# Performance work log

Hardware: AMD Instinct MI355X
Metric: run time of the kernel (lower is better)

The kernel has to match this reference:

```python
import jax, jax.numpy as jnp
import numpy as np

B, H, S, D = 4, 16, 2048, 64
NEG = -9e15


def setup_inputs() -> dict:
    key = jax.random.key(0)
    kq, kk, kv = jax.random.split(key, 3)
    q = jax.random.normal(kq, (B, H, S, D), dtype=jnp.float32)
    k = jax.random.normal(kk, (B, H, S, D), dtype=jnp.float32)
    v = jax.random.normal(kv, (B, H, S, D), dtype=jnp.float32)
    # causal mask: 1 where attention allowed, 0 where masked
    mask = jnp.tril(jnp.ones((S, S), dtype=jnp.int32))[None, None]
    return {"q": q, "k": k, "v": v, "mask": mask}


def reference(q, k, v, mask):
    d_k = q.shape[-1]
    # [B,H,S,S] scores
    scores = jnp.einsum("bhqd,bhkd->bhqk", q, k) / jnp.sqrt(jnp.float32(d_k))
    scores = jnp.where(mask == 0, jnp.float32(NEG), scores)
    attn = jax.nn.softmax(scores, axis=-1)
    return jnp.einsum("bhqk,bhkd->bhqd", attn, v)
```

## Files before the change

### kernel.cpp

```cpp
#include <hip/hip_runtime.h>

#define SLEN 2048
#define DH 64
#define NH 64
#define KVB 64
#define NT 32
#define NP 8
#define NEGBIG (-1e30f)
#define SCALE 0.18033688011112042f
#define DTHR 11.0f

typedef __attribute__((ext_vector_type(8))) short bf16x8;
typedef __attribute__((ext_vector_type(8))) unsigned short u16x8;
typedef __attribute__((ext_vector_type(16))) float f32x16;
typedef __attribute__((ext_vector_type(4))) unsigned int u32x4;

__device__ __forceinline__ ushort f2bf(float f) {
  union { float f; unsigned int u; } v; v.f = f;
  unsigned int r = v.u + 0x7fffu + ((v.u >> 16) & 1u);
  return (ushort)(r >> 16);
}

__device__ __forceinline__ unsigned int cvtpk(float lo, float hi2) {
  unsigned int r;
  asm("v_cvt_pk_bf16_f32 %0, %1, %2" : "=v"(r) : "v"(lo), "v"(hi2));
  return r;
}

__device__ __forceinline__ float xmaxh(float x) { return fmaxf(x, __shfl_xor(x, 32)); }
__device__ __forceinline__ float xsumh(float x) { return x + __shfl_xor(x, 32); }

__device__ __forceinline__ void gload16(const ushort* g, ushort* l) {
  __builtin_amdgcn_global_load_lds(
      (const __attribute__((address_space(1))) void*)g,
      (__attribute__((address_space(3))) void*)l, 16, 0, 0);
}

__global__ __launch_bounds__(256) void prep_k(const float* __restrict__ Kg,
                                              ushort* __restrict__ wsK) {
  const int tile = blockIdx.x, head = blockIdx.y, tid = threadIdx.x;
  const float* src = Kg + ((size_t)head * SLEN + (size_t)tile * KVB) * DH;
  ushort* dst = wsK + ((size_t)head * NT + tile) * (KVB * DH);
#pragma unroll
  for (int i = 0; i < 2; ++i) {
    const int id = tid + i * 256;
    const int r = id >> 3, c = id & 7;
    float4 a = *reinterpret_cast<const float4*>(src + r * DH + c * 8);
    float4 b = *reinterpret_cast<const float4*>(src + r * DH + c * 8 + 4);
    u16x8 t;
    t[0] = f2bf(a.x); t[1] = f2bf(a.y); t[2] = f2bf(a.z); t[3] = f2bf(a.w);
    t[4] = f2bf(b.x); t[5] = f2bf(b.y); t[6] = f2bf(b.z); t[7] = f2bf(b.w);
    *reinterpret_cast<u16x8*>(dst + r * DH + ((c ^ (r & 7)) * 8)) = t;
  }
}

__global__ __launch_bounds__(256) void prep_v(const float* __restrict__ Vg,
                                              ushort* __restrict__ wsV) {
  __shared__ float Vl[KVB][DH + 1];
  const int tile = blockIdx.x, head = blockIdx.y, tid = threadIdx.x;
  const float* src = Vg + ((size_t)head * SLEN + (size_t)tile * KVB) * DH;
#pragma unroll
  for (int i = 0; i < 4; ++i) {
    const int n = tid + i * 256;
    const int row = n >> 4, c4 = (n & 15) << 2;
    *reinterpret_cast<float4*>(&Vl[row][c4]) =
        *reinterpret_cast<const float4*>(src + row * DH + c4);
  }
  __syncthreads();
  ushort* dst = wsV + ((size_t)head * NT + tile) * (KVB * DH);
#pragma unroll
  for (int i = 0; i < 2; ++i) {
    const int id = tid + i * 256;
    const int d = id >> 3, c = id & 7;
    u16x8 t;
#pragma unroll
    for (int j = 0; j < 8; ++j) t[j] = f2bf(Vl[c * 8 + j][d]);
    *reinterpret_cast<u16x8*>(dst + d * DH + ((c ^ (d & 7)) * 8)) = t;
  }
}

__device__ __forceinline__ void strip_tile(
    const ushort* __restrict__ Kl, const ushort* __restrict__ Vl,
    const bf16x8* qf, f32x16& o0, f32x16& o1, float& m, float& l,
    int t, int tl, int q0, int ql, int hi) {
  f32x16 s0 = (f32x16)0.0f, s1 = (f32x16)0.0f;
#pragma unroll
  for (int ks = 0; ks < 4; ++ks) {
    const int c = ((ks * 2 + hi) ^ (ql & 7)) * 8;
    bf16x8 kf0 = *reinterpret_cast<const bf16x8*>(Kl + ql * 64 + c);
    bf16x8 kf1 = *reinterpret_cast<const bf16x8*>(Kl + (32 + ql) * 64 + c);
    s0 = __builtin_amdgcn_mfma_f32_32x32x16_bf16(kf0, qf[ks], s0, 0, 0, 0);
    s1 = __builtin_amdgcn_mfma_f32_32x32x16_bf16(kf1, qf[ks], s1, 0, 0, 0);
  }

  if (t == tl) {
    const int qg = q0 + ql;
#pragma unroll
    for (int r = 0; r < 16; ++r) {
      const int kr = t * 64 + (r & 3) + 8 * (r >> 2) + 4 * hi;
      if (kr > qg)      s0[r] = NEGBIG;
      if (kr + 32 > qg) s1[r] = NEGBIG;
    }
  }

  float tm[16];
#pragma unroll
  for (int r = 0; r < 16; ++r) tm[r] = fmaxf(s0[r], s1[r]);
#pragma unroll
  for (int st = 8; st >= 1; st >>= 1)
#pragma unroll
    for (int r = 0; r < 8; ++r)
      if (r < st) tm[r] = fmaxf(tm[r], tm[r + st]);
  const float pm = xmaxh(tm[0]);

  if (__any(pm > m + DTHR)) {
    const float mn = fmaxf(m, pm);
    const float sc = __builtin_exp2f(m - mn);
    m = mn;
    l *= sc;
#pragma unroll
    for (int r = 0; r < 16; ++r) { o0[r] *= sc; o1[r] *= sc; }
  }

#pragma unroll
  for (int r = 0; r < 16; ++r) s0[r] = __builtin_exp2f(s0[r] - m);
#pragma unroll
  for (int r = 0; r < 16; ++r) s1[r] = __builtin_exp2f(s1[r] - m);

  float ts[16];
#pragma unroll
  for (int r = 0; r < 16; ++r) ts[r] = s0[r] + s1[r];
#pragma unroll
  for (int st = 8; st >= 1; st >>= 1)
#pragma unroll
    for (int r = 0; r < 8; ++r)
      if (r < st) ts[r] += ts[r + st];
  l += xsumh(ts[0]);

  unsigned int pw0[8], pw1[8];
#pragma unroll
  for (int g = 0; g < 4; ++g)
#pragma unroll
    for (int j = 0; j < 2; ++j) {
      pw0[g * 2 + j] = cvtpk(s0[4 * g + 2 * j], s0[4 * g + 2 * j + 1]);
      pw1[g * 2 + j] = cvtpk(s1[4 * g + 2 * j], s1[4 * g + 2 * j + 1]);
    }

#pragma unroll
  for (int st = 0; st < 4; ++st) {
    const unsigned int* PW = (st < 2) ? pw0 : pw1;
    const int KH = st & 1;
    const unsigned int a0 = PW[4 * KH + 0], a1 = PW[4 * KH + 1];
    const unsigned int b0 = PW[4 * KH + 2], b1 = PW[4 * KH + 3];
    const unsigned int s0w = hi ? a0 : b0, s1w = hi ? a1 : b1;
    const unsigned int r0 = __shfl_xor(s0w, 32), r1 = __shfl_xor(s1w, 32);
    const unsigned int k0 = hi ? b0 : a0, k1 = hi ? b1 : a1;
    u32x4 fu;
    fu[0] = hi ? r0 : k0; fu[1] = hi ? r1 : k1;
    fu[2] = hi ? k0 : r0; fu[3] = hi ? k1 : r1;
    const bf16x8 pf = __builtin_bit_cast(bf16x8, fu);
    const int cv = ((st * 2 + hi) ^ (ql & 7)) * 8;
    const bf16x8 vf0 = *reinterpret_cast<const bf16x8*>(Vl + ql * 64 + cv);
    const bf16x8 vf1 = *reinterpret_cast<const bf16x8*>(Vl + (32 + ql) * 64 + cv);
    o0 = __builtin_amdgcn_mfma_f32_32x32x16_bf16(vf0, pf, o0, 0, 0, 0);
    o1 = __builtin_amdgcn_mfma_f32_32x32x16_bf16(vf1, pf, o1, 0, 0, 0);
  }
}

__device__ __forceinline__ void load_q(const float* Qh, int q0, int ql, int hi,
                                       bf16x8* qf) {
  const float* qrow = Qh + (size_t)(q0 + ql) * DH;
#pragma unroll
  for (int ks = 0; ks < 4; ++ks) {
    const int d0 = ks * 16 + hi * 8;
    float4 a = *reinterpret_cast<const float4*>(qrow + d0);
    float4 b = *reinterpret_cast<const float4*>(qrow + d0 + 4);
    bf16x8 t;
    t[0] = (short)f2bf(a.x * SCALE); t[1] = (short)f2bf(a.y * SCALE);
    t[2] = (short)f2bf(a.z * SCALE); t[3] = (short)f2bf(a.w * SCALE);
    t[4] = (short)f2bf(b.x * SCALE); t[5] = (short)f2bf(b.y * SCALE);
    t[6] = (short)f2bf(b.z * SCALE); t[7] = (short)f2bf(b.w * SCALE);
    qf[ks] = t;
  }
}

__device__ __forceinline__ void epi(float* Ow, float* Oh, const f32x16& o,
                                    float invl, int q0, int subd, int lane) {
  const int ql = lane & 31, hi = lane >> 5;
#pragma unroll
  for (int g = 0; g < 4; ++g) {
    float4 vv = make_float4(o[4 * g] * invl, o[4 * g + 1] * invl,
                            o[4 * g + 2] * invl, o[4 * g + 3] * invl);
    *reinterpret_cast<float4*>(Ow + ql * 36 + 8 * g + 4 * hi) = vv;
  }
#pragma unroll
  for (int i = 0; i < 4; ++i) {
    const int qr = (lane >> 3) + i * 8;
    const int c4 = (lane & 7) * 4;
    float4 vv = *reinterpret_cast<const float4*>(Ow + qr * 36 + c4);
    *reinterpret_cast<float4*>(Oh + (size_t)(q0 + qr) * DH + subd * 32 + c4) = vv;
  }
}

__global__ __launch_bounds__(256, 2) void attn_fwd5(
    const float* __restrict__ Qg, const ushort* __restrict__ wsK,
    const ushort* __restrict__ wsV, float* __restrict__ Og) {
  __shared__ __align__(16) float smem[8192];
  ushort* stg = (ushort*)smem;

  const int p    = blockIdx.x;
  const int head = blockIdx.y;
  const int tid  = threadIdx.x;
  const int w    = tid >> 6;
  const int lane = tid & 63;
  const int hi   = lane >> 5;
  const int ql   = lane & 31;

  const int q0A = p * 128 + w * 32;
  const int q0B = (15 - p) * 128 + w * 32;
  const int tlA = q0A >> 6;
  const int tlB = q0B >> 6;
  const int nt  = 32 - 2 * p;

  const float*  Qh    = Qg + (size_t)head * SLEN * DH;
  float*        Oh    = Og + (size_t)head * SLEN * DH;
  const ushort* kbase = wsK + (size_t)head * (NT * KVB * DH);
  const ushort* vbase = wsV + (size_t)head * (NT * KVB * DH);

#define STAGE(buf, t)                                                          \
  do {                                                                         \
    const size_t tb_ = (size_t)(t) * 4096;                                     \
    gload16(kbase + tb_ + tid * 8,        stg + (buf) * 8192 + tid * 8);       \
    gload16(kbase + tb_ + 2048 + tid * 8, stg + (buf) * 8192 + 2048 + tid * 8);\
    gload16(vbase + tb_ + tid * 8,        stg + (buf) * 8192 + 4096 + tid * 8);\
    gload16(vbase + tb_ + 2048 + tid * 8,                                      \
            stg + (buf) * 8192 + 6144 + tid * 8);                              \
  } while (0)

  STAGE(0, 0);

  bf16x8 qfA[4], qfB[4];
  load_q(Qh, q0A, ql, hi, qfA);
  load_q(Qh, q0B, ql, hi, qfB);

  f32x16 oA0 = (f32x16)0.0f, oA1 = (f32x16)0.0f;
  f32x16 oB0 = (f32x16)0.0f, oB1 = (f32x16)0.0f;
  float mA = -3.0e38f, lA = 0.0f, mB = -3.0e38f, lB = 0.0f;

  __syncthreads();

  int cur = 0;
  for (int t = 0; t < nt; ++t) {
    if (t + 1 < nt) STAGE(cur ^ 1, t + 1);

    const ushort* Kl = stg + cur * 8192;
    const ushort* Vl = Kl + 4096;

    if (t <= tlB) strip_tile(Kl, Vl, qfB, oB0, oB1, mB, lB, t, tlB, q0B, ql, hi);
    if (t <= tlA) strip_tile(Kl, Vl, qfA, oA0, oA1, mA, lA, t, tlA, q0A, ql, hi);

    __syncthreads();
    cur ^= 1;
  }
#undef STAGE

  float* Ow = smem + w * 1152;
  const float iA = 1.0f / lA, iB = 1.0f / lB;
  epi(Ow, Oh, oA0, iA, q0A, 0, lane);
  epi(Ow, Oh, oA1, iA, q0A, 1, lane);
  epi(Ow, Oh, oB0, iB, q0B, 0, lane);
  epi(Ow, Oh, oB1, iB, q0B, 1, lane);
}

extern "C" void kernel_launch(void* const* d_in, const int* in_sizes, int n_in,
                              void* d_out, int out_size, void* d_ws, size_t ws_size,
                              hipStream_t stream) {
  const float* q = (const float*)d_in[0];
  const float* k = (const float*)d_in[1];
  const float* v = (const float*)d_in[2];
  float* out = (float*)d_out;

  const size_t per = (size_t)NH * SLEN * DH;
  ushort* wsK = (ushort*)d_ws;
  ushort* wsV = wsK + per;

  prep_k<<<dim3(NT, NH), 256, 0, stream>>>(k, wsK);
  prep_v<<<dim3(NT, NH), 256, 0, stream>>>(v, wsV);
  attn_fwd5<<<dim3(NP, NH), 256, 0, stream>>>(q, wsK, wsV, out);
}
```

Measured before the change: 100.3 us.

## Split attention into 2-wave blocks with interleaved QK/softmax and MFMA priority

The attention kernel moves to 128-thread blocks, each covering a 64-row query strip paired with its mirrored strip, and launches twice as many blocks with head as the fast grid dimension. The per-tile work is split into a QK^T phase and a softmax+PV phase, so both strips' score MFMAs are issued before either softmax, and s_setprio raises wave priority around the MFMA sections. The intent is more parallelism and better overlap of matrix and vector work, at the cost of redundant K/V staging per block and extra live registers for two score tiles. The prep kernels swap grid axes to match.

```diff
diff --git a/kernel.cpp b/kernel.cpp
--- a/kernel.cpp
+++ b/kernel.cpp
@@ -5,7 +5,7 @@
 #define NH 64
 #define KVB 64
 #define NT 32
-#define NP 8
+#define NP 16
 #define NEGBIG (-1e30f)
 #define SCALE 0.18033688011112042f
 #define DTHR 11.0f
@@ -38,7 +38,7 @@
 
 __global__ __launch_bounds__(256) void prep_k(const float* __restrict__ Kg,
                                               ushort* __restrict__ wsK) {
-  const int tile = blockIdx.x, head = blockIdx.y, tid = threadIdx.x;
+  const int head = blockIdx.x, tile = blockIdx.y, tid = threadIdx.x;
   const float* src = Kg + ((size_t)head * SLEN + (size_t)tile * KVB) * DH;
   ushort* dst = wsK + ((size_t)head * NT + tile) * (KVB * DH);
 #pragma unroll
@@ -57,7 +57,7 @@
 __global__ __launch_bounds__(256) void prep_v(const float* __restrict__ Vg,
                                               ushort* __restrict__ wsV) {
   __shared__ float Vl[KVB][DH + 1];
-  const int tile = blockIdx.x, head = blockIdx.y, tid = threadIdx.x;
+  const int head = blockIdx.x, tile = blockIdx.y, tid = threadIdx.x;
   const float* src = Vg + ((size_t)head * SLEN + (size_t)tile * KVB) * DH;
 #pragma unroll
   for (int i = 0; i < 4; ++i) {
@@ -79,11 +79,11 @@
   }
 }
 
-__device__ __forceinline__ void strip_tile(
-    const ushort* __restrict__ Kl, const ushort* __restrict__ Vl,
-    const bf16x8* qf, f32x16& o0, f32x16& o1, float& m, float& l,
-    int t, int tl, int q0, int ql, int hi) {
-  f32x16 s0 = (f32x16)0.0f, s1 = (f32x16)0.0f;
+__device__ __forceinline__ void qkt(const ushort* __restrict__ Kl,
+                                    const bf16x8* qf, f32x16& s0, f32x16& s1,
+                                    int ql, int hi) {
+  s0 = (f32x16)0.0f; s1 = (f32x16)0.0f;
+  __builtin_amdgcn_s_setprio(1);
 #pragma unroll
   for (int ks = 0; ks < 4; ++ks) {
     const int c = ((ks * 2 + hi) ^ (ql & 7)) * 8;
@@ -92,7 +92,13 @@
     s0 = __builtin_amdgcn_mfma_f32_32x32x16_bf16(kf0, qf[ks], s0, 0, 0, 0);
     s1 = __builtin_amdgcn_mfma_f32_32x32x16_bf16(kf1, qf[ks], s1, 0, 0, 0);
   }
-
+  __builtin_amdgcn_s_setprio(0);
+}
+
+__device__ __forceinline__ void fin(const ushort* __restrict__ Vl,
+                                    f32x16& s0, f32x16& s1, f32x16& o0,
+                                    f32x16& o1, float& m, float& l, int t,
+                                    int tl, int q0, int ql, int hi) {
   if (t == tl) {
     const int qg = q0 + ql;
 #pragma unroll
@@ -146,6 +152,7 @@
       pw1[g * 2 + j] = cvtpk(s1[4 * g + 2 * j], s1[4 * g + 2 * j + 1]);
     }
 
+  __builtin_amdgcn_s_setprio(1);
 #pragma unroll
   for (int st = 0; st < 4; ++st) {
     const unsigned int* PW = (st < 2) ? pw0 : pw1;
@@ -165,6 +172,7 @@
     o0 = __builtin_amdgcn_mfma_f32_32x32x16_bf16(vf0, pf, o0, 0, 0, 0);
     o1 = __builtin_amdgcn_mfma_f32_32x32x16_bf16(vf1, pf, o1, 0, 0, 0);
   }
+  __builtin_amdgcn_s_setprio(0);
 }
 
 __device__ __forceinline__ void load_q(const float* Qh, int q0, int ql, int hi,
@@ -202,25 +210,25 @@
   }
 }
 
-__global__ __launch_bounds__(256, 2) void attn_fwd5(
+__global__ __launch_bounds__(128, 2) void attn_fwd6(
     const float* __restrict__ Qg, const ushort* __restrict__ wsK,
     const ushort* __restrict__ wsV, float* __restrict__ Og) {
   __shared__ __align__(16) float smem[8192];
   ushort* stg = (ushort*)smem;
 
-  const int p    = blockIdx.x;
-  const int head = blockIdx.y;
+  const int head = blockIdx.x;
+  const int p    = blockIdx.y;
   const int tid  = threadIdx.x;
   const int w    = tid >> 6;
   const int lane = tid & 63;
   const int hi   = lane >> 5;
   const int ql   = lane & 31;
 
-  const int q0A = p * 128 + w * 32;
-  const int q0B = (15 - p) * 128 + w * 32;
-  const int tlA = q0A >> 6;
-  const int tlB = q0B >> 6;
-  const int nt  = 32 - 2 * p;
+  const int q0A = p * 64 + w * 32;
+  const int q0B = (31 - p) * 64 + w * 32;
+  const int tlA = p;
+  const int tlB = 31 - p;
+  const int nt  = 32 - p;
 
   const float*  Qh    = Qg + (size_t)head * SLEN * DH;
   float*        Oh    = Og + (size_t)head * SLEN * DH;
@@ -230,11 +238,13 @@
 #define STAGE(buf, t)                                                          \
   do {                                                                         \
     const size_t tb_ = (size_t)(t) * 4096;                                     \
-    gload16(kbase + tb_ + tid * 8,        stg + (buf) * 8192 + tid * 8);       \
-    gload16(kbase + tb_ + 2048 + tid * 8, stg + (buf) * 8192 + 2048 + tid * 8);\
-    gload16(vbase + tb_ + tid * 8,        stg + (buf) * 8192 + 4096 + tid * 8);\
-    gload16(vbase + tb_ + 2048 + tid * 8,                                      \
-            stg + (buf) * 8192 + 6144 + tid * 8);                              \
+    _Pragma("unroll")                                                          \
+    for (int j_ = 0; j_ < 4; ++j_) {                                           \
+      gload16(kbase + tb_ + j_ * 1024 + tid * 8,                               \
+              stg + (buf) * 8192 + j_ * 1024 + tid * 8);                       \
+      gload16(vbase + tb_ + j_ * 1024 + tid * 8,                               \
+              stg + (buf) * 8192 + 4096 + j_ * 1024 + tid * 8);                \
+    }                                                                          \
   } while (0)
 
   STAGE(0, 0);
@@ -255,9 +265,13 @@
 
     const ushort* Kl = stg + cur * 8192;
     const ushort* Vl = Kl + 4096;
-
-    if (t <= tlB) strip_tile(Kl, Vl, qfB, oB0, oB1, mB, lB, t, tlB, q0B, ql, hi);
-    if (t <= tlA) strip_tile(Kl, Vl, qfA, oA0, oA1, mA, lA, t, tlA, q0A, ql, hi);
+    const bool doA = (t <= tlA);
+
+    f32x16 sB0, sB1, sA0, sA1;
+    qkt(Kl, qfB, sB0, sB1, ql, hi);
+    if (doA) qkt(Kl, qfA, sA0, sA1, ql, hi);
+    fin(Vl, sB0, sB1, oB0, oB1, mB, lB, t, tlB, q0B, ql, hi);
+    if (doA) fin(Vl, sA0, sA1, oA0, oA1, mA, lA, t, tlA, q0A, ql, hi);
 
     __syncthreads();
     cur ^= 1;
@@ -284,7 +298,7 @@
   ushort* wsK = (ushort*)d_ws;
   ushort* wsV = wsK + per;
 
-  prep_k<<<dim3(NT, NH), 256, 0, stream>>>(k, wsK);
-  prep_v<<<dim3(NT, NH), 256, 0, stream>>>(v, wsV);
-  attn_fwd5<<<dim3(NP, NH), 256, 0, stream>>>(q, wsK, wsV, out);
-}
+  prep_k<<<dim3(NH, NT), 256, 0, stream>>>(k, wsK);
+  prep_v<<<dim3(NH, NT), 256, 0, stream>>>(v, wsV);
+  attn_fwd6<<<dim3(NH, NP), 128, 0, stream>>>(q, wsK, wsV, out);
+}
```

Measured after the change: 100.7 us. About the same (+0.4%).
